# Kernel optimization log

Measured on AMD Instinct MI355X. Metric: run time of the kernel, lower is better.

The kernel has to match this reference:

```python
import jax, jax.numpy as jnp
import numpy as np

B, N, D = 4, 4096, 1024
EPS = 1e-5


def layer_norm(x, g, b):
    mu = jnp.mean(x, axis=-1, keepdims=True)
    var = jnp.mean(jnp.square(x - mu), axis=-1, keepdims=True)
    return (x - mu) * jax.lax.rsqrt(var + EPS) * g + b


def expert(x, w1, b1, w2, b2, scalar, lng, lnb):
    h = jax.nn.gelu(jnp.einsum('bnd,fd->bnf', x, w1) + b1, approximate=False)
    y = jnp.einsum('bnf,df->bnd', h, w2) + b2
    return layer_norm(x + y * scalar, lng, lnb)


def setup_inputs() -> dict:
    key = jax.random.key(0)
    ks = jax.random.split(key, 16)
    d = {
        'x': jax.random.normal(ks[0], (B, N, D), dtype=jnp.float32),
        'weights': jax.random.normal(ks[1], (1, 1, N), dtype=jnp.float32) * 0.02,
        'norm_g': jnp.ones((D,), jnp.float32),
        'norm_b': jnp.zeros((D,), jnp.float32),
    }
    for i in range(2):
        o = 2 + 4 * i
        d[f'w1_{i}'] = jax.random.normal(ks[o], (4 * D, D), jnp.float32) * (1.0 / np.sqrt(D))
        d[f'b1_{i}'] = jnp.zeros((4 * D,), jnp.float32)
        d[f'w2_{i}'] = jax.random.normal(ks[o + 1], (D, 4 * D), jnp.float32) * (1.0 / np.sqrt(4 * D))
        d[f'b2_{i}'] = jnp.zeros((D,), jnp.float32)
        d[f's_{i}'] = jax.random.normal(ks[o + 2], (1,), jnp.float32) * 0.1
        d[f'lng_{i}'] = jnp.ones((D,), jnp.float32)
        d[f'lnb_{i}'] = jnp.zeros((D,), jnp.float32)
    return d


def reference(x, weights, norm_g, norm_b,
              w1_0, b1_0, w2_0, b2_0, s_0, lng_0, lnb_0,
              w1_1, b1_1, w2_1, b2_1, s_1, lng_1, lnb_1):
    n = x.shape[1]
    # FFT long-conv token mixing: x -> [B, D, N], circular conv with length-2N zero padding
    xt = jnp.transpose(x, (0, 2, 1))
    xf = jnp.fft.fft(xt, n=2 * n)
    wf = jnp.fft.fft(weights, n=2 * n)
    y = jnp.fft.ifft(xf * wf).real[..., :n]
    y = jnp.transpose(y, (0, 2, 1))  # [B, N, D]
    scale = jnp.sqrt(1.0 / (jnp.arange(n, dtype=jnp.float32) + 1.0))[None, :, None]
    x1 = layer_norm(x + y * scale, norm_g, norm_b)
    h0, h1 = jnp.split(x1, 2, axis=1)
    o0 = expert(h0, w1_0, b1_0, w2_0, b2_0, s_0, lng_0, lnb_0)
    o1 = expert(h1, w1_1, b1_1, w2_1, b2_1, s_1, lng_1, lnb_1)
    return jnp.concatenate([o0, o1], axis=1)
```

## Files before the change

kernel.cpp:

```cpp
#include <hip/hip_runtime.h>
#include <math.h>

typedef unsigned short u16;
typedef unsigned int u32;

using bf16x8 = __attribute__((ext_vector_type(8))) short;
using f32x4  = __attribute__((ext_vector_type(4))) float;

__device__ __forceinline__ u16 f2bf(float f) {
  u32 u = __float_as_uint(f);
  u32 r = u + 0x7FFFu + ((u >> 16) & 1u);
  return (u16)(r >> 16);
}
__device__ __forceinline__ float bf2f(u16 h) {
  return __uint_as_float(((u32)h) << 16);
}

__device__ __forceinline__ void gll16(const u16* g, u16* l) {
  __builtin_amdgcn_global_load_lds((const __attribute__((address_space(1))) void*)g,
                                   (__attribute__((address_space(3))) void*)l, 16, 0, 0);
}

__global__ __launch_bounds__(256) void k_split(const float* __restrict__ src,
                                               u16* __restrict__ h) {
  size_t i = ((size_t)blockIdx.x << 8) + threadIdx.x;
  float4 v = *(const float4*)(src + (i << 2));
  ushort4 hv;
  hv.x = f2bf(v.x);
  hv.y = f2bf(v.y);
  hv.z = f2bf(v.z);
  hv.w = f2bf(v.w);
  *(ushort4*)(h + (i << 2)) = hv;
}

__global__ __launch_bounds__(256) void k_wsplit(const float* __restrict__ w,
                                                u16* __restrict__ wrh8) {
  int bid = blockIdx.x;
  int p = bid / 17;
  int i = (bid % 17) * 256 + threadIdx.x;
  int j = i + p;
  float v = (j <= 4095) ? w[4095 - j] : 0.0f;
  wrh8[(size_t)p * 4352 + i] = f2bf(v);
}

__global__ __launch_bounds__(256) void k_tsplit(const float* __restrict__ x,
                                                u16* __restrict__ Xth) {
  __shared__ float tile[64 * 65];
  int bid = blockIdx.x;
  int b = bid >> 10; int rem = bid & 1023;
  int mt = rem >> 4; int dt = rem & 15;
  int m0 = mt << 6, d0 = dt << 6;
  int tid = threadIdx.x;
  int rr = tid >> 4, cc = (tid & 15) << 2;
#pragma unroll
  for (int i = 0; i < 4; i++) {
    int r = (i << 4) + rr;
    float4 v = *(const float4*)(x + (size_t)(b * 4096 + m0 + r) * 1024 + d0 + cc);
    tile[r * 65 + cc + 0] = v.x; tile[r * 65 + cc + 1] = v.y;
    tile[r * 65 + cc + 2] = v.z; tile[r * 65 + cc + 3] = v.w;
  }
  __syncthreads();
#pragma unroll
  for (int i = 0; i < 4; i++) {
    int rd = (i << 4) + rr;
    ushort4 hv;
    hv.x = f2bf(tile[(cc + 0) * 65 + rd]);
    hv.y = f2bf(tile[(cc + 1) * 65 + rd]);
    hv.z = f2bf(tile[(cc + 2) * 65 + rd]);
    hv.w = f2bf(tile[(cc + 3) * 65 + rd]);
    size_t o = (size_t)(b * 1024 + d0 + rd) * 4096 + m0 + cc;
    *(ushort4*)(Xth + o) = hv;
  }
}

__global__ __launch_bounds__(256) void k_convm(const u16* __restrict__ Xth,
                                               const u16* __restrict__ wrh8,
                                               const float* __restrict__ x,
                                               float* __restrict__ U) {
  __shared__ __align__(16) u16 Ash[128 * 32], Bsh[128 * 32];
  int bid = blockIdx.x;
  int nt = 31 - (bid >> 5);
  int b  = (bid >> 3) & 3;
  int dt = bid & 7;
  int n0 = nt << 7, d0 = dt << 7;
  int tid = threadIdx.x, lane = tid & 63, w4 = tid >> 6;
  int wm = w4 >> 1, wn = w4 & 1;
  const u16* Xbh = Xth + (size_t)b * 4194304;
  f32x4 acc[4][4];
#pragma unroll
  for (int i = 0; i < 4; i++)
#pragma unroll
    for (int j = 0; j < 4; j++) { acc[i][j][0] = 0.f; acc[i][j][1] = 0.f; acc[i][j][2] = 0.f; acc[i][j][3] = 0.f; }
  int arow0 = (wm << 6) + (lane & 15);
  int brow0 = (wn << 6) + (lane & 15);
  int koff = (lane >> 4) << 3;
  int kIters = (nt << 2) + 4;
  for (int it = 0; it < kIters; ++it) {
    int m0 = it << 5;
    int C = 4095 - n0 + m0;
#pragma unroll
    for (int c = 0; c < 2; ++c) {
      int s = (c << 8) + tid;
      int r = s >> 2, kq = s & 3;
      int lb = (s & ~63) << 3;
      int base = C - r;
      int p = base & 7;
      size_t ao = (size_t)p * 4352 + (base - p) + (kq << 3);
      gll16(wrh8 + ao, Ash + lb);
      size_t go = (size_t)(d0 + r) * 4096 + m0 + (kq << 3);
      gll16(Xbh + go, Bsh + lb);
    }
    __syncthreads();
    bf16x8 af[4], bfh[4];
#pragma unroll
    for (int i = 0; i < 4; i++)
      af[i] = *(const bf16x8*)(Ash + (arow0 + (i << 4)) * 32 + koff);
#pragma unroll
    for (int j = 0; j < 4; j++)
      bfh[j] = *(const bf16x8*)(Bsh + (brow0 + (j << 4)) * 32 + koff);
#pragma unroll
    for (int i = 0; i < 4; i++)
#pragma unroll
      for (int j = 0; j < 4; j++)
        acc[i][j] = __builtin_amdgcn_mfma_f32_16x16x32_bf16(af[i], bfh[j], acc[i][j], 0, 0, 0);
    __syncthreads();
  }
#pragma unroll
  for (int i = 0; i < 4; i++) {
    int nb_ = n0 + (wm << 6) + (i << 4) + ((lane >> 4) << 2);
#pragma unroll
    for (int q = 0; q < 4; q++) {
      int n = nb_ + q;
      float scale = rsqrtf((float)(n + 1));
#pragma unroll
      for (int j = 0; j < 4; j++) {
        int d = d0 + (wn << 6) + (j << 4) + (lane & 15);
        size_t idx = ((size_t)(b * 4096 + n)) * 1024 + d;
        U[idx] = x[idx] + acc[i][j][q] * scale;
      }
    }
  }
}

__device__ __forceinline__ float blk_sum(float v, float* sb, int tid) {
#pragma unroll
  for (int off = 32; off > 0; off >>= 1) v += __shfl_down(v, off, 64);
  int wid = tid >> 6;
  if ((tid & 63) == 0) sb[wid] = v;
  __syncthreads();
  if (tid == 0) sb[4] = sb[0] + sb[1] + sb[2] + sb[3];
  __syncthreads();
  return sb[4];
}

__global__ __launch_bounds__(256) void k_ln1b(const float* __restrict__ U,
                                              const float* __restrict__ g,
                                              const float* __restrict__ bt,
                                              u16* __restrict__ X1h,
                                              u16* __restrict__ X1l) {
  __shared__ float sb[8];
  int row = blockIdx.x; int tid = threadIdx.x;
  int c = tid << 2;
  float4 v = *(const float4*)(U + (size_t)row * 1024 + c);
  float mu = blk_sum(v.x + v.y + v.z + v.w, sb, tid) * (1.0f / 1024.0f);
  float dx = v.x - mu, dy = v.y - mu, dz = v.z - mu, dw = v.w - mu;
  float var = blk_sum(dx * dx + dy * dy + dz * dz + dw * dw, sb, tid) * (1.0f / 1024.0f);
  float rs = 1.0f / sqrtf(var + 1e-5f);
  float4 gv = *(const float4*)(g + c);
  float4 bv = *(const float4*)(bt + c);
  float o0 = dx * rs * gv.x + bv.x;
  float o1 = dy * rs * gv.y + bv.y;
  float o2 = dz * rs * gv.z + bv.z;
  float o3 = dw * rs * gv.w + bv.w;
  ushort4 hv, lv;
  hv.x = f2bf(o0); lv.x = f2bf(o0 - bf2f(hv.x));
  hv.y = f2bf(o1); lv.y = f2bf(o1 - bf2f(hv.y));
  hv.z = f2bf(o2); lv.z = f2bf(o2 - bf2f(hv.z));
  hv.w = f2bf(o3); lv.w = f2bf(o3 - bf2f(hv.w));
  *(ushort4*)(X1h + (size_t)row * 1024 + c) = hv;
  *(ushort4*)(X1l + (size_t)row * 1024 + c) = lv;
}

__global__ __launch_bounds__(256) void k_ffn1m(const u16* __restrict__ X1h,
                                               const u16* __restrict__ W1h,
                                               const float* __restrict__ b1a, const float* __restrict__ b1b,
                                               u16* __restrict__ Hch, int e) {
  __shared__ __align__(16) u16 Ash[128 * 32], Bsh[128 * 32];
  int bid = blockIdx.x;
  int mt = bid >> 5, ct = bid & 31;
  int chunk = mt >> 4, rloc = mt & 15;
  size_t arow0g = (size_t)chunk * 4096 + (size_t)e * 2048 + (size_t)rloc * 128;
  int hrow0 = mt << 7;
  const u16* Bh = W1h + (size_t)e * 4194304;
  const float* b1 = e ? b1b : b1a;
  int tid = threadIdx.x, lane = tid & 63, w = tid >> 6;
  int wm = w >> 1, wn = w & 1;
  int col0 = ct << 7;
  f32x4 acc[4][4];
#pragma unroll
  for (int i = 0; i < 4; i++)
#pragma unroll
    for (int j = 0; j < 4; j++) { acc[i][j][0] = 0.f; acc[i][j][1] = 0.f; acc[i][j][2] = 0.f; acc[i][j][3] = 0.f; }
  int arow0 = (wm << 6) + (lane & 15);
  int brow0 = (wn << 6) + (lane & 15);
  int koff = (lane >> 4) << 3;
  for (int kt = 0; kt < 32; ++kt) {
    int k0 = kt << 5;
#pragma unroll
    for (int c = 0; c < 2; ++c) {
      int s = (c << 8) + tid;
      int r = s >> 2, kq = s & 3;
      int lb = (s & ~63) << 3;
      gll16(X1h + (arow0g + r) * 1024 + k0 + (kq << 3), Ash + lb);
      gll16(Bh + (size_t)(col0 + r) * 1024 + k0 + (kq << 3), Bsh + lb);
    }
    __syncthreads();
    bf16x8 af[4], bfh[4];
#pragma unroll
    for (int i = 0; i < 4; i++)
      af[i] = *(const bf16x8*)(Ash + (arow0 + (i << 4)) * 32 + koff);
#pragma unroll
    for (int j = 0; j < 4; j++)
      bfh[j] = *(const bf16x8*)(Bsh + (brow0 + (j << 4)) * 32 + koff);
#pragma unroll
    for (int i = 0; i < 4; i++)
#pragma unroll
      for (int j = 0; j < 4; j++)
        acc[i][j] = __builtin_amdgcn_mfma_f32_16x16x32_bf16(af[i], bfh[j], acc[i][j], 0, 0, 0);
    __syncthreads();
  }
#pragma unroll
  for (int j = 0; j < 4; j++) {
    int f = col0 + (wn << 6) + (j << 4) + (lane & 15);
    float bv = b1[f];
#pragma unroll
    for (int i = 0; i < 4; i++) {
      int rb = hrow0 + (wm << 6) + (i << 4) + ((lane >> 4) << 2);
#pragma unroll
      for (int q = 0; q < 4; q++) {
        float v = acc[i][j][q] + bv;
        float ge = 0.5f * v * (1.0f + erff(v * 0.70710678118654752f));
        Hch[(size_t)(rb + q) * 4096 + f] = f2bf(ge);
      }
    }
  }
}

__global__ __launch_bounds__(128) void k_ffn2m(const u16* __restrict__ Hch,
                                               const u16* __restrict__ W2h,
                                               u16* __restrict__ Yb, int e) {
  __shared__ __align__(16) u16 Ash[128 * 32], Bsh[64 * 32];
  int bid = blockIdx.x;
  int mt = bid >> 4, ct = bid & 15;
  int chunk = mt >> 4, rloc = mt & 15;
  int arow0h = mt << 7;
  size_t yrow0g = (size_t)chunk * 4096 + (size_t)e * 2048 + (size_t)rloc * 128;
  const u16* Bh = W2h + (size_t)e * 4194304;
  int tid = threadIdx.x, lane = tid & 63, w = tid >> 6;
  int col0 = ct << 6;
  f32x4 acc[4][4];
#pragma unroll
  for (int i = 0; i < 4; i++)
#pragma unroll
    for (int j = 0; j < 4; j++) { acc[i][j][0] = 0.f; acc[i][j][1] = 0.f; acc[i][j][2] = 0.f; acc[i][j][3] = 0.f; }
  int arow0 = (w << 6) + (lane & 15);
  int brow0 = (lane & 15);
  int koff = (lane >> 4) << 3;
  for (int kt = 0; kt < 128; ++kt) {
    int k0 = kt << 5;
#pragma unroll
    for (int c = 0; c < 4; ++c) {
      int s = (c << 7) + tid;
      int r = s >> 2, kq = s & 3;
      int lb = (s & ~63) << 3;
      gll16(Hch + (size_t)(arow0h + r) * 4096 + k0 + (kq << 3), Ash + lb);
    }
#pragma unroll
    for (int c = 0; c < 2; ++c) {
      int s = (c << 7) + tid;
      int r = s >> 2, kq = s & 3;
      int lb = (s & ~63) << 3;
      gll16(Bh + (size_t)(col0 + r) * 4096 + k0 + (kq << 3), Bsh + lb);
    }
    __syncthreads();
    bf16x8 af[4], bfh[4];
#pragma unroll
    for (int i = 0; i < 4; i++)
      af[i] = *(const bf16x8*)(Ash + (arow0 + (i << 4)) * 32 + koff);
#pragma unroll
    for (int j = 0; j < 4; j++)
      bfh[j] = *(const bf16x8*)(Bsh + (brow0 + (j << 4)) * 32 + koff);
#pragma unroll
    for (int i = 0; i < 4; i++)
#pragma unroll
      for (int j = 0; j < 4; j++)
        acc[i][j] = __builtin_amdgcn_mfma_f32_16x16x32_bf16(af[i], bfh[j], acc[i][j], 0, 0, 0);
    __syncthreads();
  }
#pragma unroll
  for (int i = 0; i < 4; i++) {
    size_t rb = yrow0g + (w << 6) + (i << 4) + ((lane >> 4) << 2);
#pragma unroll
    for (int j = 0; j < 4; j++) {
      int d = col0 + (j << 4) + (lane & 15);
#pragma unroll
      for (int q = 0; q < 4; q++)
        Yb[(rb + q) * 1024 + d] = f2bf(acc[i][j][q]);
    }
  }
}

__global__ __launch_bounds__(256) void k_ln2b(const u16* __restrict__ Yb,
                                              const u16* __restrict__ X1h, const u16* __restrict__ X1l,
                                              const float* __restrict__ b2a, const float* __restrict__ b2b,
                                              const float* __restrict__ sa, const float* __restrict__ sbp,
                                              const float* __restrict__ ga, const float* __restrict__ gb,
                                              const float* __restrict__ ba, const float* __restrict__ bbp,
                                              float* __restrict__ out) {
  __shared__ float sb[8];
  int row = blockIdx.x; int tid = threadIdx.x;
  int n = row & 4095; int e = n >> 11;
  const float* b2 = e ? b2b : b2a;
  const float* lg = e ? gb : ga;
  const float* lb = e ? bbp : ba;
  float s = e ? sbp[0] : sa[0];
  int c = tid << 2;
  ushort4 yv = *(const ushort4*)(Yb + (size_t)row * 1024 + c);
  ushort4 hv = *(const ushort4*)(X1h + (size_t)row * 1024 + c);
  ushort4 lv = *(const ushort4*)(X1l + (size_t)row * 1024 + c);
  float4 b2v = *(const float4*)(b2 + c);
  float x0 = bf2f(hv.x) + bf2f(lv.x);
  float x1 = bf2f(hv.y) + bf2f(lv.y);
  float x2 = bf2f(hv.z) + bf2f(lv.z);
  float x3 = bf2f(hv.w) + bf2f(lv.w);
  float t0 = x0 + s * (bf2f(yv.x) + b2v.x);
  float t1 = x1 + s * (bf2f(yv.y) + b2v.y);
  float t2 = x2 + s * (bf2f(yv.z) + b2v.z);
  float t3 = x3 + s * (bf2f(yv.w) + b2v.w);
  float mu = blk_sum(t0 + t1 + t2 + t3, sb, tid) * (1.0f / 1024.0f);
  float d0 = t0 - mu, d1 = t1 - mu, d2 = t2 - mu, d3 = t3 - mu;
  float var = blk_sum(d0 * d0 + d1 * d1 + d2 * d2 + d3 * d3, sb, tid) * (1.0f / 1024.0f);
  float rs = 1.0f / sqrtf(var + 1e-5f);
  float4 gv = *(const float4*)(lg + c);
  float4 bv = *(const float4*)(lb + c);
  float4 o;
  o.x = d0 * rs * gv.x + bv.x;
  o.y = d1 * rs * gv.y + bv.y;
  o.z = d2 * rs * gv.z + bv.z;
  o.w = d3 * rs * gv.w + bv.w;
  *(float4*)(out + (size_t)row * 1024 + c) = o;
}

extern "C" void kernel_launch(void* const* d_in, const int* in_sizes, int n_in,
                              void* d_out, int out_size, void* d_ws, size_t ws_size,
                              hipStream_t stream) {
  (void)out_size; (void)ws_size;
  static const int SIG[18] = {16777216, 4096, 1024, 1024,
                              4194304, 4096, 4194304, 1024, 1, 1024, 1024,
                              4194304, 4096, 4194304, 1024, 1, 1024, 1024};
  const void* P[18];
  bool exact = (n_in >= 18);
  if (exact) {
    for (int i = 0; i < 18; i++) {
      if (in_sizes[i] != SIG[i]) { exact = false; break; }
    }
  }
  if (exact) {
    for (int i = 0; i < 18; i++) P[i] = d_in[i];
  } else {
    bool used[64] = {false};
    int cap = (n_in < 64) ? n_in : 64;
    for (int r = 0; r < 18; r++) {
      int found = -1;
      for (int j = 0; j < cap; j++) {
        if (!used[j] && in_sizes[j] == SIG[r]) { found = j; break; }
      }
      if (found >= 0) { used[found] = true; P[r] = d_in[found]; }
      else            { P[r] = d_in[(r < n_in) ? r : 0]; }
    }
  }
  const float* x     = (const float*)P[0];
  const float* wv    = (const float*)P[1];
  const float* ng    = (const float*)P[2];
  const float* nb    = (const float*)P[3];
  const float* w1_0  = (const float*)P[4];
  const float* b1_0  = (const float*)P[5];
  const float* w2_0  = (const float*)P[6];
  const float* b2_0  = (const float*)P[7];
  const float* s_0   = (const float*)P[8];
  const float* lng_0 = (const float*)P[9];
  const float* lnb_0 = (const float*)P[10];
  const float* w1_1  = (const float*)P[11];
  const float* b1_1  = (const float*)P[12];
  const float* w2_1  = (const float*)P[13];
  const float* b2_1  = (const float*)P[14];
  const float* s_1   = (const float*)P[15];
  const float* lng_1 = (const float*)P[16];
  const float* lnb_1 = (const float*)P[17];

  char* ws = (char*)d_ws;
  u16* W1h = (u16*)(ws + 0);
  u16* W2h = (u16*)(ws + 16777216);
  u16* Xth = (u16*)(ws + 33554432);
  u16* X1h = Xth;
  u16* X1l = (u16*)(ws + 67108864);
  float* U = (float*)(ws + 100663296);
  u16* Hch = (u16*)(ws + 100663296);
  u16* Yb  = (u16*)(ws + 167772160);
  u16* wrh8 = (u16*)(ws + 201326592);

  k_wsplit<<<136, 256, 0, stream>>>(wv, wrh8);
  k_tsplit<<<4096, 256, 0, stream>>>(x, Xth);
  k_split<<<4096, 256, 0, stream>>>(w1_0, W1h);
  k_split<<<4096, 256, 0, stream>>>(w1_1, W1h + 4194304);
  k_split<<<4096, 256, 0, stream>>>(w2_0, W2h);
  k_split<<<4096, 256, 0, stream>>>(w2_1, W2h + 4194304);
  k_convm<<<1024, 256, 0, stream>>>(Xth, wrh8, x, U);
  k_ln1b<<<16384, 256, 0, stream>>>(U, ng, nb, X1h, X1l);
  for (int e = 0; e < 2; e++) {
    k_ffn1m<<<2048, 256, 0, stream>>>(X1h, W1h, b1_0, b1_1, Hch, e);
    k_ffn2m<<<1024, 128, 0, stream>>>(Hch, W2h, Yb, e);
  }
  k_ln2b<<<16384, 256, 0, stream>>>(Yb, X1h, X1l, b2_0, b2_1, s_0, s_1,
                                    lng_0, lng_1, lnb_0, lnb_1, (float*)d_out);
}
```

Before: 801.9 us.

## Use k-major LDS layout, stage GEMM epilogues via LDS, widen ffn2 tile

Changes the LDS tile layout in the three MFMA GEMMs from row-major 32-wide rows to k-chunk-major (8 elements per row per k-quarter), which is meant to cut LDS bank conflicts on the bf16x8 fragment reads. The ffn1 and ffn2 epilogues now stage bf16 results through padded shared memory, one half-tile at a time, and write 16-byte coalesced rows instead of scattered 2-byte stores. ffn2 moves from a 128x64 tile with 128 threads to a 128x128 tile with 256 threads and a 2x2 wave grid, halving the grid size. In exchange the epilogues gain extra barriers, and the larger ffn2 tile means fewer blocks to spread across the GPU.

```diff
diff --git a/kernel.cpp b/kernel.cpp
--- a/kernel.cpp
+++ b/kernel.cpp
@@ -77,7 +77,9 @@
                                                const u16* __restrict__ wrh8,
                                                const float* __restrict__ x,
                                                float* __restrict__ U) {
-  __shared__ __align__(16) u16 Ash[128 * 32], Bsh[128 * 32];
+  __shared__ __align__(16) u16 smem[8192];
+  u16* Ash = smem;
+  u16* Bsh = smem + 4096;
   int bid = blockIdx.x;
   int nt = 31 - (bid >> 5);
   int b  = (bid >> 3) & 3;
@@ -93,7 +95,7 @@
     for (int j = 0; j < 4; j++) { acc[i][j][0] = 0.f; acc[i][j][1] = 0.f; acc[i][j][2] = 0.f; acc[i][j][3] = 0.f; }
   int arow0 = (wm << 6) + (lane & 15);
   int brow0 = (wn << 6) + (lane & 15);
-  int koff = (lane >> 4) << 3;
+  int koff = (lane >> 4) << 10;
   int kIters = (nt << 2) + 4;
   for (int it = 0; it < kIters; ++it) {
     int m0 = it << 5;
@@ -101,7 +103,7 @@
 #pragma unroll
     for (int c = 0; c < 2; ++c) {
       int s = (c << 8) + tid;
-      int r = s >> 2, kq = s & 3;
+      int r = s & 127, kq = s >> 7;
       int lb = (s & ~63) << 3;
       int base = C - r;
       int p = base & 7;
@@ -114,10 +116,10 @@
     bf16x8 af[4], bfh[4];
 #pragma unroll
     for (int i = 0; i < 4; i++)
-      af[i] = *(const bf16x8*)(Ash + (arow0 + (i << 4)) * 32 + koff);
+      af[i] = *(const bf16x8*)(Ash + koff + ((arow0 + (i << 4)) << 3));
 #pragma unroll
     for (int j = 0; j < 4; j++)
-      bfh[j] = *(const bf16x8*)(Bsh + (brow0 + (j << 4)) * 32 + koff);
+      bfh[j] = *(const bf16x8*)(Bsh + koff + ((brow0 + (j << 4)) << 3));
 #pragma unroll
     for (int i = 0; i < 4; i++)
 #pragma unroll
@@ -185,7 +187,9 @@
                                                const u16* __restrict__ W1h,
                                                const float* __restrict__ b1a, const float* __restrict__ b1b,
                                                u16* __restrict__ Hch, int e) {
-  __shared__ __align__(16) u16 Ash[128 * 32], Bsh[128 * 32];
+  __shared__ __align__(16) u16 smem[8448];
+  u16* Ash = smem;
+  u16* Bsh = smem + 4096;
   int bid = blockIdx.x;
   int mt = bid >> 5, ct = bid & 31;
   int chunk = mt >> 4, rloc = mt & 15;
@@ -203,13 +207,13 @@
     for (int j = 0; j < 4; j++) { acc[i][j][0] = 0.f; acc[i][j][1] = 0.f; acc[i][j][2] = 0.f; acc[i][j][3] = 0.f; }
   int arow0 = (wm << 6) + (lane & 15);
   int brow0 = (wn << 6) + (lane & 15);
-  int koff = (lane >> 4) << 3;
+  int koff = (lane >> 4) << 10;
   for (int kt = 0; kt < 32; ++kt) {
     int k0 = kt << 5;
 #pragma unroll
     for (int c = 0; c < 2; ++c) {
       int s = (c << 8) + tid;
-      int r = s >> 2, kq = s & 3;
+      int r = s & 127, kq = s >> 7;
       int lb = (s & ~63) << 3;
       gll16(X1h + (arow0g + r) * 1024 + k0 + (kq << 3), Ash + lb);
       gll16(Bh + (size_t)(col0 + r) * 1024 + k0 + (kq << 3), Bsh + lb);
@@ -218,10 +222,10 @@
     bf16x8 af[4], bfh[4];
 #pragma unroll
     for (int i = 0; i < 4; i++)
-      af[i] = *(const bf16x8*)(Ash + (arow0 + (i << 4)) * 32 + koff);
+      af[i] = *(const bf16x8*)(Ash + koff + ((arow0 + (i << 4)) << 3));
 #pragma unroll
     for (int j = 0; j < 4; j++)
-      bfh[j] = *(const bf16x8*)(Bsh + (brow0 + (j << 4)) * 32 + koff);
+      bfh[j] = *(const bf16x8*)(Bsh + koff + ((brow0 + (j << 4)) << 3));
 #pragma unroll
     for (int i = 0; i < 4; i++)
 #pragma unroll
@@ -230,66 +234,77 @@
     __syncthreads();
   }
 #pragma unroll
-  for (int j = 0; j < 4; j++) {
-    int f = col0 + (wn << 6) + (j << 4) + (lane & 15);
-    float bv = b1[f];
-#pragma unroll
-    for (int i = 0; i < 4; i++) {
-      int rb = hrow0 + (wm << 6) + (i << 4) + ((lane >> 4) << 2);
-#pragma unroll
-      for (int q = 0; q < 4; q++) {
-        float v = acc[i][j][q] + bv;
-        float ge = 0.5f * v * (1.0f + erff(v * 0.70710678118654752f));
-        Hch[(size_t)(rb + q) * 4096 + f] = f2bf(ge);
+  for (int p = 0; p < 2; ++p) {
+    if (wm == p) {
+#pragma unroll
+      for (int j = 0; j < 4; j++) {
+        int fl = (wn << 6) + (j << 4) + (lane & 15);
+        float bv = b1[col0 + fl];
+#pragma unroll
+        for (int i = 0; i < 4; i++) {
+          int rl = (i << 4) + ((lane >> 4) << 2);
+#pragma unroll
+          for (int q = 0; q < 4; q++) {
+            float v = acc[i][j][q] + bv;
+            float ge = 0.5f * v * (1.0f + erff(v * 0.70710678118654752f));
+            smem[(rl + q) * 132 + fl] = f2bf(ge);
+          }
+        }
       }
     }
-  }
-}
-
-__global__ __launch_bounds__(128) void k_ffn2m(const u16* __restrict__ Hch,
+    __syncthreads();
+#pragma unroll
+    for (int v = 0; v < 4; v++) {
+      int idx = (v << 8) + tid;
+      int row = idx >> 4, cq = idx & 15;
+      bf16x8 val = *(const bf16x8*)(smem + row * 132 + (cq << 3));
+      *(bf16x8*)(Hch + (size_t)(hrow0 + (p << 6) + row) * 4096 + col0 + (cq << 3)) = val;
+    }
+    __syncthreads();
+  }
+}
+
+__global__ __launch_bounds__(256) void k_ffn2m(const u16* __restrict__ Hch,
                                                const u16* __restrict__ W2h,
                                                u16* __restrict__ Yb, int e) {
-  __shared__ __align__(16) u16 Ash[128 * 32], Bsh[64 * 32];
+  __shared__ __align__(16) u16 smem[8448];
+  u16* Ash = smem;
+  u16* Bsh = smem + 4096;
   int bid = blockIdx.x;
-  int mt = bid >> 4, ct = bid & 15;
+  int mt = bid >> 3, ct = bid & 7;
   int chunk = mt >> 4, rloc = mt & 15;
   int arow0h = mt << 7;
   size_t yrow0g = (size_t)chunk * 4096 + (size_t)e * 2048 + (size_t)rloc * 128;
   const u16* Bh = W2h + (size_t)e * 4194304;
   int tid = threadIdx.x, lane = tid & 63, w = tid >> 6;
-  int col0 = ct << 6;
+  int wm = w >> 1, wn = w & 1;
+  int col0 = ct << 7;
   f32x4 acc[4][4];
 #pragma unroll
   for (int i = 0; i < 4; i++)
 #pragma unroll
     for (int j = 0; j < 4; j++) { acc[i][j][0] = 0.f; acc[i][j][1] = 0.f; acc[i][j][2] = 0.f; acc[i][j][3] = 0.f; }
-  int arow0 = (w << 6) + (lane & 15);
-  int brow0 = (lane & 15);
-  int koff = (lane >> 4) << 3;
+  int arow0 = (wm << 6) + (lane & 15);
+  int brow0 = (wn << 6) + (lane & 15);
+  int koff = (lane >> 4) << 10;
   for (int kt = 0; kt < 128; ++kt) {
     int k0 = kt << 5;
 #pragma unroll
-    for (int c = 0; c < 4; ++c) {
-      int s = (c << 7) + tid;
-      int r = s >> 2, kq = s & 3;
+    for (int c = 0; c < 2; ++c) {
+      int s = (c << 8) + tid;
+      int r = s & 127, kq = s >> 7;
       int lb = (s & ~63) << 3;
       gll16(Hch + (size_t)(arow0h + r) * 4096 + k0 + (kq << 3), Ash + lb);
-    }
-#pragma unroll
-    for (int c = 0; c < 2; ++c) {
-      int s = (c << 7) + tid;
-      int r = s >> 2, kq = s & 3;
-      int lb = (s & ~63) << 3;
       gll16(Bh + (size_t)(col0 + r) * 4096 + k0 + (kq << 3), Bsh + lb);
     }
     __syncthreads();
     bf16x8 af[4], bfh[4];
 #pragma unroll
     for (int i = 0; i < 4; i++)
-      af[i] = *(const bf16x8*)(Ash + (arow0 + (i << 4)) * 32 + koff);
+      af[i] = *(const bf16x8*)(Ash + koff + ((arow0 + (i << 4)) << 3));
 #pragma unroll
     for (int j = 0; j < 4; j++)
-      bfh[j] = *(const bf16x8*)(Bsh + (brow0 + (j << 4)) * 32 + koff);
+      bfh[j] = *(const bf16x8*)(Bsh + koff + ((brow0 + (j << 4)) << 3));
 #pragma unroll
     for (int i = 0; i < 4; i++)
 #pragma unroll
@@ -298,15 +313,29 @@
     __syncthreads();
   }
 #pragma unroll
-  for (int i = 0; i < 4; i++) {
-    size_t rb = yrow0g + (w << 6) + (i << 4) + ((lane >> 4) << 2);
-#pragma unroll
-    for (int j = 0; j < 4; j++) {
-      int d = col0 + (j << 4) + (lane & 15);
-#pragma unroll
-      for (int q = 0; q < 4; q++)
-        Yb[(rb + q) * 1024 + d] = f2bf(acc[i][j][q]);
-    }
+  for (int p = 0; p < 2; ++p) {
+    if (wm == p) {
+#pragma unroll
+      for (int j = 0; j < 4; j++) {
+        int fl = (wn << 6) + (j << 4) + (lane & 15);
+#pragma unroll
+        for (int i = 0; i < 4; i++) {
+          int rl = (i << 4) + ((lane >> 4) << 2);
+#pragma unroll
+          for (int q = 0; q < 4; q++)
+            smem[(rl + q) * 132 + fl] = f2bf(acc[i][j][q]);
+        }
+      }
+    }
+    __syncthreads();
+#pragma unroll
+    for (int v = 0; v < 4; v++) {
+      int idx = (v << 8) + tid;
+      int row = idx >> 4, cq = idx & 15;
+      bf16x8 val = *(const bf16x8*)(smem + row * 132 + (cq << 3));
+      *(bf16x8*)(Yb + (yrow0g + (p << 6) + row) * 1024 + col0 + (cq << 3)) = val;
+    }
+    __syncthreads();
   }
 }
 
@@ -419,7 +448,7 @@
   k_ln1b<<<16384, 256, 0, stream>>>(U, ng, nb, X1h, X1l);
   for (int e = 0; e < 2; e++) {
     k_ffn1m<<<2048, 256, 0, stream>>>(X1h, W1h, b1_0, b1_1, Hch, e);
-    k_ffn2m<<<1024, 128, 0, stream>>>(Hch, W2h, Yb, e);
+    k_ffn2m<<<512, 256, 0, stream>>>(Hch, W2h, Yb, e);
   }
   k_ln2b<<<16384, 256, 0, stream>>>(Yb, X1h, X1l, b2_0, b2_1, s_0, s_1,
                                     lng_0, lng_1, lnb_0, lnb_1, (float*)d_out);
```

Result: slower. 1.230 ms (+53.3%).
